# Kernel tuning notes

Hardware: AMD Instinct MI355X
Metric: run time of the kernel (lower is better)

The kernel has to match this reference:

```python
import jax, jax.numpy as jnp
import numpy as np

N_NODES = 50000
N_EDGES = 800000
D_IN = 64
F1 = 64
F2 = 64
D_HID = 100


def setup_inputs() -> dict:
    key = jax.random.key(0)
    ks = jax.random.split(key, 12)
    x = jax.random.normal(ks[0], (N_NODES, D_IN), dtype=jnp.float32)
    edge_src = jax.random.randint(ks[1], (N_EDGES,), 0, N_NODES, dtype=jnp.int32)
    edge_dst = jax.random.randint(ks[2], (N_EDGES,), 0, N_NODES, dtype=jnp.int32)
    # stands in for pre-normalized GCN adjacency values (D^-1/2 (A+I) D^-1/2)
    edge_weight = jax.random.uniform(ks[3], (N_EDGES,), dtype=jnp.float32)
    def glorot(k, shape):
        lim = np.sqrt(6.0 / (shape[0] + shape[1]))
        return jax.random.uniform(k, shape, jnp.float32, -lim, lim)
    W1 = glorot(ks[4], (D_IN, F1))
    b1 = jnp.zeros((F1,), jnp.float32)
    W2 = glorot(ks[5], (F1, F2))
    b2 = jnp.zeros((F2,), jnp.float32)
    Wd = glorot(ks[6], (F2, D_HID))
    bd = jnp.zeros((D_HID,), jnp.float32)
    Wo = glorot(ks[7], (D_HID, 1))
    bo = jnp.zeros((1,), jnp.float32)
    return {"x": x, "edge_src": edge_src, "edge_dst": edge_dst,
            "edge_weight": edge_weight, "W1": W1, "b1": b1, "W2": W2,
            "b2": b2, "Wd": Wd, "bd": bd, "Wo": Wo, "bo": bo}


def _gcn_conv(x, edge_src, edge_dst, edge_weight, W, b):
    # spektral GCNConv: out = swish(A_norm @ (X @ W) + b)
    h = x @ W                                        # [N, F]
    msg = h[edge_src] * edge_weight[:, None]          # [E, F] gather + scale
    agg = jax.ops.segment_sum(msg, edge_dst, num_segments=N_NODES)  # [N, F]
    return jax.nn.swish(agg + b)


def reference(x, edge_src, edge_dst, edge_weight, W1, b1, W2, b2, Wd, bd, Wo, bo):
    h = _gcn_conv(x, edge_src, edge_dst, edge_weight, W1, b1)
    h = _gcn_conv(h, edge_src, edge_dst, edge_weight, W2, b2)
    h = jax.nn.swish(h @ Wd + bd)                    # Dense(100, swish)
    return jax.nn.sigmoid(h @ Wo + bo)               # Dense(1, sigmoid) -> [N, 1]
```

## Files before the change

### kernel.cpp

```cpp
#include <hip/hip_runtime.h>
#include <hip/hip_fp16.h>

#define N_NODES 50000
#define N_EDGES 800000
#define D 64
#define DHID 100
#define NTILES (N_NODES / 16)
#define NCT 7
#define CAP 64
#define FILL_BLOCKS ((N_EDGES + 255) / 256)
#define MM_BLOCKS ((NTILES + 3) / 4)

typedef unsigned short ushort;
typedef unsigned int uint;
typedef __attribute__((ext_vector_type(8))) short s16x8;
typedef __attribute__((ext_vector_type(4))) float f32x4;

#define MFMA16(A, B, C) __builtin_amdgcn_mfma_f32_16x16x32_bf16((A), (B), (C), 0, 0, 0)

__device__ __forceinline__ float swishf(float x) { return x / (1.0f + __expf(-x)); }

__device__ __forceinline__ ushort f2bf(float f) {
    uint u = __float_as_uint(f);
    uint r = (u + 0x7fffu + ((u >> 16) & 1u)) >> 16;
    return (ushort)r;
}
__device__ __forceinline__ float bf2f(ushort h) { return __uint_as_float((uint)h << 16); }
__device__ __forceinline__ float bf_lo(uint d) { return __uint_as_float(d << 16); }
__device__ __forceinline__ float bf_hi(uint d) { return __uint_as_float(d & 0xffff0000u); }

__device__ __forceinline__ void accum8(float* acc, uint4 v, float w) {
    acc[0] = fmaf(w, bf_lo(v.x), acc[0]);
    acc[1] = fmaf(w, bf_hi(v.x), acc[1]);
    acc[2] = fmaf(w, bf_lo(v.y), acc[2]);
    acc[3] = fmaf(w, bf_hi(v.y), acc[3]);
    acc[4] = fmaf(w, bf_lo(v.z), acc[4]);
    acc[5] = fmaf(w, bf_hi(v.z), acc[5]);
    acc[6] = fmaf(w, bf_lo(v.w), acc[6]);
    acc[7] = fmaf(w, bf_hi(v.w), acc[7]);
}

__global__ __launch_bounds__(256) void fill_and_l1(const int* __restrict__ src,
                                                   const int* __restrict__ dst,
                                                   const float* __restrict__ w,
                                                   int* __restrict__ degPad,
                                                   uint* __restrict__ csr,
                                                   const float* __restrict__ X,
                                                   const float* __restrict__ W,
                                                   ushort* __restrict__ H) {
    __shared__ __align__(16) short sBT[2][D][72];
    __shared__ __align__(16) short rep[4][16][72];
    int tid = threadIdx.x;

    if (blockIdx.x < FILL_BLOCKS) {
        int e = blockIdx.x * 256 + tid;
        if (e < N_EDGES) {
            int d = dst[e];
            uint hw = (uint)__half_as_ushort(__float2half_rn(w[e]));
            uint payload = (uint)src[e] | (hw << 16);
            int r = atomicAdd(&degPad[d << 4], 1);
            r = min(r, CAP - 1);
            csr[(d << 6) + r] = payload;
        }
        return;
    }

    for (int idx = tid; idx < D * D; idx += 256) {
        int k = idx >> 6, c = idx & 63;
        float wv = W[idx];
        ushort hi = f2bf(wv);
        ushort lo = f2bf(wv - bf2f(hi));
        sBT[0][c][k] = (short)hi;
        sBT[1][c][k] = (short)lo;
    }
    __syncthreads();
    int wv_ = tid >> 6, lane = tid & 63, quad = lane >> 4, m = lane & 15;
    int tile = (blockIdx.x - FILL_BLOCKS) * 4 + wv_;
    if (tile >= NTILES) return;
    int node0 = tile * 16;

    f32x4 acc[4] = {{0,0,0,0},{0,0,0,0},{0,0,0,0},{0,0,0,0}};
#pragma unroll
    for (int kt = 0; kt < 2; ++kt) {
        int k0 = kt * 32 + quad * 8;
        const float* xp = X + ((size_t)(node0 + m) << 6) + k0;
        float4 xa = *((const float4*)xp);
        float4 xb = *((const float4*)(xp + 4));
        float xv[8] = {xa.x, xa.y, xa.z, xa.w, xb.x, xb.y, xb.z, xb.w};
        s16x8 ahi, alo;
#pragma unroll
        for (int jj = 0; jj < 8; ++jj) {
            ushort hi = f2bf(xv[jj]);
            ahi[jj] = (short)hi;
            alo[jj] = (short)f2bf(xv[jj] - bf2f(hi));
        }
#pragma unroll
        for (int ct = 0; ct < 4; ++ct) {
            int n = ct * 16 + m;
            s16x8 bhi = *((const s16x8*)&sBT[0][n][k0]);
            s16x8 blo = *((const s16x8*)&sBT[1][n][k0]);
            acc[ct] = MFMA16(ahi, bhi, acc[ct]);
            acc[ct] = MFMA16(ahi, blo, acc[ct]);
            acc[ct] = MFMA16(alo, bhi, acc[ct]);
        }
    }
#pragma unroll
    for (int ct = 0; ct < 4; ++ct)
#pragma unroll
        for (int r = 0; r < 4; ++r)
            rep[wv_][quad * 4 + r][ct * 16 + m] = (short)f2bf(acc[ct][r]);
#pragma unroll
    for (int half = 0; half < 2; ++half) {
        int r = (lane >> 3) + half * 8;
        int c0 = (lane & 7) * 8;
        s16x8 v = *((const s16x8*)&rep[wv_][r][c0]);
        *((s16x8*)(H + ((size_t)(node0 + r) << 6) + c0)) = v;
    }
}

__global__ __launch_bounds__(256) void mfma_l2(const ushort* __restrict__ act,
                                               const float* __restrict__ W,
                                               ushort* __restrict__ H) {
    __shared__ __align__(16) short sBT[2][D][72];
    __shared__ __align__(16) short rep[4][16][72];
    int tid = threadIdx.x;
    for (int idx = tid; idx < D * D; idx += 256) {
        int k = idx >> 6, c = idx & 63;
        float wv = W[idx];
        ushort hi = f2bf(wv);
        ushort lo = f2bf(wv - bf2f(hi));
        sBT[0][c][k] = (short)hi;
        sBT[1][c][k] = (short)lo;
    }
    __syncthreads();
    int w = tid >> 6, lane = tid & 63, quad = lane >> 4, m = lane & 15;
    int tile = blockIdx.x * 4 + w;
    if (tile >= NTILES) return;
    int node0 = tile * 16;

    f32x4 acc[4] = {{0,0,0,0},{0,0,0,0},{0,0,0,0},{0,0,0,0}};
#pragma unroll
    for (int kt = 0; kt < 2; ++kt) {
        int k0 = kt * 32 + quad * 8;
        s16x8 a = *((const s16x8*)(act + ((size_t)(node0 + m) << 6) + k0));
#pragma unroll
        for (int ct = 0; ct < 4; ++ct) {
            int n = ct * 16 + m;
            s16x8 bhi = *((const s16x8*)&sBT[0][n][k0]);
            s16x8 blo = *((const s16x8*)&sBT[1][n][k0]);
            acc[ct] = MFMA16(a, bhi, acc[ct]);
            acc[ct] = MFMA16(a, blo, acc[ct]);
        }
    }
#pragma unroll
    for (int ct = 0; ct < 4; ++ct)
#pragma unroll
        for (int r = 0; r < 4; ++r)
            rep[w][quad * 4 + r][ct * 16 + m] = (short)f2bf(acc[ct][r]);
#pragma unroll
    for (int half = 0; half < 2; ++half) {
        int r = (lane >> 3) + half * 8;
        int c0 = (lane & 7) * 8;
        s16x8 v = *((const s16x8*)&rep[w][r][c0]);
        *((s16x8*)(H + ((size_t)(node0 + r) << 6) + c0)) = v;
    }
}

__global__ __launch_bounds__(256) void gather_act(const ushort* __restrict__ H,
                                                  const int* __restrict__ degPad,
                                                  const uint* __restrict__ csr,
                                                  const float* __restrict__ bias,
                                                  ushort* __restrict__ actOut) {
    int tid = threadIdx.x;
    int wave = tid >> 6, lane = tid & 63;
    int j = lane >> 3, fg = lane & 7;
    int node = blockIdx.x * 4 + wave;
    int cnt = (degPad[node << 4] + 31) & ~31;
    const uint* bucket = csr + ((size_t)node << 6);

    float acc[8] = {0, 0, 0, 0, 0, 0, 0, 0};
    for (int base = 0; base < cnt; base += 32) {
        int i0 = base + j;
        uint e0 = bucket[i0];
        uint e1 = bucket[i0 + 8];
        uint e2 = bucket[i0 + 16];
        uint e3 = bucket[i0 + 24];
        float w0 = __half2float(__ushort_as_half((ushort)(e0 >> 16)));
        float w1 = __half2float(__ushort_as_half((ushort)(e1 >> 16)));
        float w2 = __half2float(__ushort_as_half((ushort)(e2 >> 16)));
        float w3 = __half2float(__ushort_as_half((ushort)(e3 >> 16)));
        uint4 v0 = *((const uint4*)(H + ((size_t)(e0 & 0xffffu) << 6) + (fg << 3)));
        uint4 v1 = *((const uint4*)(H + ((size_t)(e1 & 0xffffu) << 6) + (fg << 3)));
        uint4 v2 = *((const uint4*)(H + ((size_t)(e2 & 0xffffu) << 6) + (fg << 3)));
        uint4 v3 = *((const uint4*)(H + ((size_t)(e3 & 0xffffu) << 6) + (fg << 3)));
        accum8(acc, v0, w0);
        accum8(acc, v1, w1);
        accum8(acc, v2, w2);
        accum8(acc, v3, w3);
    }
#pragma unroll
    for (int t = 0; t < 8; ++t) {
        acc[t] += __shfl_xor(acc[t], 8, 64);
        acc[t] += __shfl_xor(acc[t], 16, 64);
        acc[t] += __shfl_xor(acc[t], 32, 64);
    }
    if (j == 0) {
        float4 ba = ((const float4*)bias)[fg * 2];
        float4 bb = ((const float4*)bias)[fg * 2 + 1];
        float r0 = swishf(acc[0] + ba.x);
        float r1 = swishf(acc[1] + ba.y);
        float r2 = swishf(acc[2] + ba.z);
        float r3 = swishf(acc[3] + ba.w);
        float r4 = swishf(acc[4] + bb.x);
        float r5 = swishf(acc[5] + bb.y);
        float r6 = swishf(acc[6] + bb.z);
        float r7 = swishf(acc[7] + bb.w);
        uint4 u;
        u.x = (uint)f2bf(r0) | ((uint)f2bf(r1) << 16);
        u.y = (uint)f2bf(r2) | ((uint)f2bf(r3) << 16);
        u.z = (uint)f2bf(r4) | ((uint)f2bf(r5) << 16);
        u.w = (uint)f2bf(r6) | ((uint)f2bf(r7) << 16);
        *((uint4*)(actOut + ((size_t)node << 6) + (fg << 3))) = u;
    }
}

__global__ __launch_bounds__(256) void mfma_head(const ushort* __restrict__ act2,
                                                 const float* __restrict__ Wd,
                                                 const float* __restrict__ bd,
                                                 const float* __restrict__ Wo,
                                                 const float* __restrict__ bo,
                                                 float* __restrict__ out) {
    __shared__ __align__(16) short sBT[2][NCT * 16][72];
    __shared__ float sbd[NCT * 16];
    __shared__ float sWo[NCT * 16];
    int tid = threadIdx.x;
    for (int idx = tid; idx < NCT * 16 * D; idx += 256) {
        int jj = idx >> 6, k = idx & 63;
        float wv = (jj < DHID) ? Wd[k * DHID + jj] : 0.f;
        ushort hi = f2bf(wv);
        ushort lo = f2bf(wv - bf2f(hi));
        sBT[0][jj][k] = (short)hi;
        sBT[1][jj][k] = (short)lo;
    }
    if (tid < NCT * 16) {
        sbd[tid] = (tid < DHID) ? bd[tid] : 0.f;
        sWo[tid] = (tid < DHID) ? Wo[tid] : 0.f;
    }
    __syncthreads();
    int w = tid >> 6, lane = tid & 63, quad = lane >> 4, m = lane & 15;
    int tile = blockIdx.x * 4 + w;
    if (tile >= NTILES) return;
    int node0 = tile * 16;

    f32x4 acc[NCT];
#pragma unroll
    for (int ct = 0; ct < NCT; ++ct) acc[ct] = (f32x4){0, 0, 0, 0};
#pragma unroll
    for (int kt = 0; kt < 2; ++kt) {
        int k0 = kt * 32 + quad * 8;
        s16x8 a = *((const s16x8*)(act2 + ((size_t)(node0 + m) << 6) + k0));
#pragma unroll
        for (int ct = 0; ct < NCT; ++ct) {
            int n = ct * 16 + m;
            s16x8 bhi = *((const s16x8*)&sBT[0][n][k0]);
            s16x8 blo = *((const s16x8*)&sBT[1][n][k0]);
            acc[ct] = MFMA16(a, bhi, acc[ct]);
            acc[ct] = MFMA16(a, blo, acc[ct]);
        }
    }
    float part[4] = {0, 0, 0, 0};
#pragma unroll
    for (int ct = 0; ct < NCT; ++ct) {
        int jj = ct * 16 + m;
        float bdv = sbd[jj], wov = sWo[jj];
#pragma unroll
        for (int r = 0; r < 4; ++r)
            part[r] = fmaf(swishf(acc[ct][r] + bdv), wov, part[r]);
    }
#pragma unroll
    for (int r = 0; r < 4; ++r) {
        part[r] += __shfl_xor(part[r], 1, 64);
        part[r] += __shfl_xor(part[r], 2, 64);
        part[r] += __shfl_xor(part[r], 4, 64);
        part[r] += __shfl_xor(part[r], 8, 64);
    }
    if (m == 0) {
        float b0 = bo[0];
        float4 o;
        o.x = 1.f / (1.f + __expf(-(part[0] + b0)));
        o.y = 1.f / (1.f + __expf(-(part[1] + b0)));
        o.z = 1.f / (1.f + __expf(-(part[2] + b0)));
        o.w = 1.f / (1.f + __expf(-(part[3] + b0)));
        *((float4*)(out + node0 + quad * 4)) = o;
    }
}

extern "C" void kernel_launch(void* const* d_in, const int* in_sizes, int n_in,
                              void* d_out, int out_size, void* d_ws, size_t ws_size,
                              hipStream_t stream) {
    const float* x   = (const float*)d_in[0];
    const int* esrc  = (const int*)d_in[1];
    const int* edst  = (const int*)d_in[2];
    const float* ew  = (const float*)d_in[3];
    const float* W1  = (const float*)d_in[4];
    const float* b1  = (const float*)d_in[5];
    const float* W2  = (const float*)d_in[6];
    const float* b2  = (const float*)d_in[7];
    const float* Wd  = (const float*)d_in[8];
    const float* bd  = (const float*)d_in[9];
    const float* Wo  = (const float*)d_in[10];
    const float* bo  = (const float*)d_in[11];
    float* out = (float*)d_out;

    char* ws = (char*)d_ws;
    ushort* H1   = (ushort*)ws;  ws += (size_t)N_NODES * D * sizeof(ushort);
    ushort* act1 = (ushort*)ws;  ws += (size_t)N_NODES * D * sizeof(ushort);
    ushort* H2   = (ushort*)ws;  ws += (size_t)N_NODES * D * sizeof(ushort);
    ushort* act2 = (ushort*)ws;  ws += (size_t)N_NODES * D * sizeof(ushort);
    uint* csr    = (uint*)ws;    ws += (size_t)N_NODES * CAP * sizeof(uint);
    int* degPad  = (int*)ws;     ws += (size_t)N_NODES * 16 * sizeof(int);

    const int gBlocks = N_NODES / 4;

    hipMemsetAsync(csr, 0, (size_t)N_NODES * (CAP + 16) * sizeof(uint), stream);

    fill_and_l1<<<FILL_BLOCKS + MM_BLOCKS, 256, 0, stream>>>(esrc, edst, ew, degPad, csr,
                                                             x, W1, H1);

    gather_act<<<gBlocks, 256, 0, stream>>>(H1, degPad, csr, b1, act1);

    mfma_l2<<<(NTILES + 3) / 4, 256, 0, stream>>>(act1, W2, H2);
    gather_act<<<gBlocks, 256, 0, stream>>>(H2, degPad, csr, b2, act2);

    mfma_head<<<(NTILES + 3) / 4, 256, 0, stream>>>(act2, Wd, bd, Wo, bo, out);
}
```

Before: 215.3 us.

## Fuse all stages into one persistent cooperative kernel with grid syncs

Replaces the memset and five separate kernel launches with a single cooperative persistent kernel. Inside it, grid.sync separates the stages: zeroing, edge bucketing plus layer-1 matmul, gather, layer-2 matmul, gather, and the head. Degree counters are packed densely instead of padded to 16 ints each. This removes launch gaps and the separate memset, at the cost of grid-wide barriers, fewer resident waves during the latency-bound gather stages, and occupancy capped by the shared-memory and register use of the fused kernel.

```diff
diff --git a/kernel.cpp b/kernel.cpp
--- a/kernel.cpp
+++ b/kernel.cpp
@@ -1,5 +1,8 @@
 #include <hip/hip_runtime.h>
 #include <hip/hip_fp16.h>
+#include <hip/hip_cooperative_groups.h>
+
+namespace cg = cooperative_groups;
 
 #define N_NODES 50000
 #define N_EDGES 800000
@@ -8,8 +11,7 @@
 #define NTILES (N_NODES / 16)
 #define NCT 7
 #define CAP 64
-#define FILL_BLOCKS ((N_EDGES + 255) / 256)
-#define MM_BLOCKS ((NTILES + 3) / 4)
+#define ZERO_UINT4 812500
 
 typedef unsigned short ushort;
 typedef unsigned int uint;
@@ -40,258 +42,270 @@
     acc[7] = fmaf(w, bf_hi(v.w), acc[7]);
 }
 
-__global__ __launch_bounds__(256) void fill_and_l1(const int* __restrict__ src,
-                                                   const int* __restrict__ dst,
-                                                   const float* __restrict__ w,
-                                                   int* __restrict__ degPad,
-                                                   uint* __restrict__ csr,
-                                                   const float* __restrict__ X,
-                                                   const float* __restrict__ W,
-                                                   ushort* __restrict__ H) {
-    __shared__ __align__(16) short sBT[2][D][72];
-    __shared__ __align__(16) short rep[4][16][72];
-    int tid = threadIdx.x;
-
-    if (blockIdx.x < FILL_BLOCKS) {
-        int e = blockIdx.x * 256 + tid;
-        if (e < N_EDGES) {
-            int d = dst[e];
-            uint hw = (uint)__half_as_ushort(__float2half_rn(w[e]));
-            uint payload = (uint)src[e] | (hw << 16);
-            int r = atomicAdd(&degPad[d << 4], 1);
-            r = min(r, CAP - 1);
-            csr[(d << 6) + r] = payload;
-        }
-        return;
-    }
-
-    for (int idx = tid; idx < D * D; idx += 256) {
-        int k = idx >> 6, c = idx & 63;
-        float wv = W[idx];
-        ushort hi = f2bf(wv);
-        ushort lo = f2bf(wv - bf2f(hi));
-        sBT[0][c][k] = (short)hi;
-        sBT[1][c][k] = (short)lo;
-    }
-    __syncthreads();
-    int wv_ = tid >> 6, lane = tid & 63, quad = lane >> 4, m = lane & 15;
-    int tile = (blockIdx.x - FILL_BLOCKS) * 4 + wv_;
-    if (tile >= NTILES) return;
-    int node0 = tile * 16;
-
-    f32x4 acc[4] = {{0,0,0,0},{0,0,0,0},{0,0,0,0},{0,0,0,0}};
-#pragma unroll
-    for (int kt = 0; kt < 2; ++kt) {
-        int k0 = kt * 32 + quad * 8;
-        const float* xp = X + ((size_t)(node0 + m) << 6) + k0;
-        float4 xa = *((const float4*)xp);
-        float4 xb = *((const float4*)(xp + 4));
-        float xv[8] = {xa.x, xa.y, xa.z, xa.w, xb.x, xb.y, xb.z, xb.w};
-        s16x8 ahi, alo;
-#pragma unroll
-        for (int jj = 0; jj < 8; ++jj) {
-            ushort hi = f2bf(xv[jj]);
-            ahi[jj] = (short)hi;
-            alo[jj] = (short)f2bf(xv[jj] - bf2f(hi));
-        }
-#pragma unroll
-        for (int ct = 0; ct < 4; ++ct) {
-            int n = ct * 16 + m;
-            s16x8 bhi = *((const s16x8*)&sBT[0][n][k0]);
-            s16x8 blo = *((const s16x8*)&sBT[1][n][k0]);
-            acc[ct] = MFMA16(ahi, bhi, acc[ct]);
-            acc[ct] = MFMA16(ahi, blo, acc[ct]);
-            acc[ct] = MFMA16(alo, bhi, acc[ct]);
-        }
-    }
-#pragma unroll
-    for (int ct = 0; ct < 4; ++ct)
-#pragma unroll
-        for (int r = 0; r < 4; ++r)
-            rep[wv_][quad * 4 + r][ct * 16 + m] = (short)f2bf(acc[ct][r]);
-#pragma unroll
-    for (int half = 0; half < 2; ++half) {
-        int r = (lane >> 3) + half * 8;
-        int c0 = (lane & 7) * 8;
-        s16x8 v = *((const s16x8*)&rep[wv_][r][c0]);
-        *((s16x8*)(H + ((size_t)(node0 + r) << 6) + c0)) = v;
-    }
-}
-
-__global__ __launch_bounds__(256) void mfma_l2(const ushort* __restrict__ act,
-                                               const float* __restrict__ W,
-                                               ushort* __restrict__ H) {
-    __shared__ __align__(16) short sBT[2][D][72];
-    __shared__ __align__(16) short rep[4][16][72];
-    int tid = threadIdx.x;
-    for (int idx = tid; idx < D * D; idx += 256) {
-        int k = idx >> 6, c = idx & 63;
-        float wv = W[idx];
-        ushort hi = f2bf(wv);
-        ushort lo = f2bf(wv - bf2f(hi));
-        sBT[0][c][k] = (short)hi;
-        sBT[1][c][k] = (short)lo;
-    }
-    __syncthreads();
-    int w = tid >> 6, lane = tid & 63, quad = lane >> 4, m = lane & 15;
-    int tile = blockIdx.x * 4 + w;
-    if (tile >= NTILES) return;
-    int node0 = tile * 16;
-
-    f32x4 acc[4] = {{0,0,0,0},{0,0,0,0},{0,0,0,0},{0,0,0,0}};
-#pragma unroll
-    for (int kt = 0; kt < 2; ++kt) {
-        int k0 = kt * 32 + quad * 8;
-        s16x8 a = *((const s16x8*)(act + ((size_t)(node0 + m) << 6) + k0));
-#pragma unroll
-        for (int ct = 0; ct < 4; ++ct) {
-            int n = ct * 16 + m;
-            s16x8 bhi = *((const s16x8*)&sBT[0][n][k0]);
-            s16x8 blo = *((const s16x8*)&sBT[1][n][k0]);
-            acc[ct] = MFMA16(a, bhi, acc[ct]);
-            acc[ct] = MFMA16(a, blo, acc[ct]);
-        }
-    }
-#pragma unroll
-    for (int ct = 0; ct < 4; ++ct)
-#pragma unroll
-        for (int r = 0; r < 4; ++r)
-            rep[w][quad * 4 + r][ct * 16 + m] = (short)f2bf(acc[ct][r]);
-#pragma unroll
-    for (int half = 0; half < 2; ++half) {
-        int r = (lane >> 3) + half * 8;
-        int c0 = (lane & 7) * 8;
-        s16x8 v = *((const s16x8*)&rep[w][r][c0]);
-        *((s16x8*)(H + ((size_t)(node0 + r) << 6) + c0)) = v;
-    }
-}
-
-__global__ __launch_bounds__(256) void gather_act(const ushort* __restrict__ H,
-                                                  const int* __restrict__ degPad,
-                                                  const uint* __restrict__ csr,
-                                                  const float* __restrict__ bias,
-                                                  ushort* __restrict__ actOut) {
-    int tid = threadIdx.x;
-    int wave = tid >> 6, lane = tid & 63;
+__device__ __forceinline__ void gather_stage(const ushort* __restrict__ H,
+                                             const int* __restrict__ deg,
+                                             const uint* __restrict__ csr,
+                                             const float* __restrict__ bias,
+                                             ushort* __restrict__ actOut,
+                                             int waveslot, int nslots, int lane) {
     int j = lane >> 3, fg = lane & 7;
-    int node = blockIdx.x * 4 + wave;
-    int cnt = (degPad[node << 4] + 31) & ~31;
-    const uint* bucket = csr + ((size_t)node << 6);
-
-    float acc[8] = {0, 0, 0, 0, 0, 0, 0, 0};
-    for (int base = 0; base < cnt; base += 32) {
-        int i0 = base + j;
-        uint e0 = bucket[i0];
-        uint e1 = bucket[i0 + 8];
-        uint e2 = bucket[i0 + 16];
-        uint e3 = bucket[i0 + 24];
-        float w0 = __half2float(__ushort_as_half((ushort)(e0 >> 16)));
-        float w1 = __half2float(__ushort_as_half((ushort)(e1 >> 16)));
-        float w2 = __half2float(__ushort_as_half((ushort)(e2 >> 16)));
-        float w3 = __half2float(__ushort_as_half((ushort)(e3 >> 16)));
-        uint4 v0 = *((const uint4*)(H + ((size_t)(e0 & 0xffffu) << 6) + (fg << 3)));
-        uint4 v1 = *((const uint4*)(H + ((size_t)(e1 & 0xffffu) << 6) + (fg << 3)));
-        uint4 v2 = *((const uint4*)(H + ((size_t)(e2 & 0xffffu) << 6) + (fg << 3)));
-        uint4 v3 = *((const uint4*)(H + ((size_t)(e3 & 0xffffu) << 6) + (fg << 3)));
-        accum8(acc, v0, w0);
-        accum8(acc, v1, w1);
-        accum8(acc, v2, w2);
-        accum8(acc, v3, w3);
-    }
-#pragma unroll
-    for (int t = 0; t < 8; ++t) {
-        acc[t] += __shfl_xor(acc[t], 8, 64);
-        acc[t] += __shfl_xor(acc[t], 16, 64);
-        acc[t] += __shfl_xor(acc[t], 32, 64);
-    }
-    if (j == 0) {
-        float4 ba = ((const float4*)bias)[fg * 2];
-        float4 bb = ((const float4*)bias)[fg * 2 + 1];
-        float r0 = swishf(acc[0] + ba.x);
-        float r1 = swishf(acc[1] + ba.y);
-        float r2 = swishf(acc[2] + ba.z);
-        float r3 = swishf(acc[3] + ba.w);
-        float r4 = swishf(acc[4] + bb.x);
-        float r5 = swishf(acc[5] + bb.y);
-        float r6 = swishf(acc[6] + bb.z);
-        float r7 = swishf(acc[7] + bb.w);
-        uint4 u;
-        u.x = (uint)f2bf(r0) | ((uint)f2bf(r1) << 16);
-        u.y = (uint)f2bf(r2) | ((uint)f2bf(r3) << 16);
-        u.z = (uint)f2bf(r4) | ((uint)f2bf(r5) << 16);
-        u.w = (uint)f2bf(r6) | ((uint)f2bf(r7) << 16);
-        *((uint4*)(actOut + ((size_t)node << 6) + (fg << 3))) = u;
-    }
-}
-
-__global__ __launch_bounds__(256) void mfma_head(const ushort* __restrict__ act2,
-                                                 const float* __restrict__ Wd,
-                                                 const float* __restrict__ bd,
-                                                 const float* __restrict__ Wo,
-                                                 const float* __restrict__ bo,
-                                                 float* __restrict__ out) {
-    __shared__ __align__(16) short sBT[2][NCT * 16][72];
-    __shared__ float sbd[NCT * 16];
-    __shared__ float sWo[NCT * 16];
-    int tid = threadIdx.x;
-    for (int idx = tid; idx < NCT * 16 * D; idx += 256) {
-        int jj = idx >> 6, k = idx & 63;
-        float wv = (jj < DHID) ? Wd[k * DHID + jj] : 0.f;
-        ushort hi = f2bf(wv);
-        ushort lo = f2bf(wv - bf2f(hi));
-        sBT[0][jj][k] = (short)hi;
-        sBT[1][jj][k] = (short)lo;
-    }
-    if (tid < NCT * 16) {
-        sbd[tid] = (tid < DHID) ? bd[tid] : 0.f;
-        sWo[tid] = (tid < DHID) ? Wo[tid] : 0.f;
-    }
-    __syncthreads();
-    int w = tid >> 6, lane = tid & 63, quad = lane >> 4, m = lane & 15;
-    int tile = blockIdx.x * 4 + w;
-    if (tile >= NTILES) return;
-    int node0 = tile * 16;
-
-    f32x4 acc[NCT];
-#pragma unroll
-    for (int ct = 0; ct < NCT; ++ct) acc[ct] = (f32x4){0, 0, 0, 0};
-#pragma unroll
-    for (int kt = 0; kt < 2; ++kt) {
-        int k0 = kt * 32 + quad * 8;
-        s16x8 a = *((const s16x8*)(act2 + ((size_t)(node0 + m) << 6) + k0));
-#pragma unroll
-        for (int ct = 0; ct < NCT; ++ct) {
-            int n = ct * 16 + m;
-            s16x8 bhi = *((const s16x8*)&sBT[0][n][k0]);
-            s16x8 blo = *((const s16x8*)&sBT[1][n][k0]);
-            acc[ct] = MFMA16(a, bhi, acc[ct]);
-            acc[ct] = MFMA16(a, blo, acc[ct]);
-        }
-    }
-    float part[4] = {0, 0, 0, 0};
-#pragma unroll
-    for (int ct = 0; ct < NCT; ++ct) {
-        int jj = ct * 16 + m;
-        float bdv = sbd[jj], wov = sWo[jj];
-#pragma unroll
-        for (int r = 0; r < 4; ++r)
-            part[r] = fmaf(swishf(acc[ct][r] + bdv), wov, part[r]);
-    }
-#pragma unroll
-    for (int r = 0; r < 4; ++r) {
-        part[r] += __shfl_xor(part[r], 1, 64);
-        part[r] += __shfl_xor(part[r], 2, 64);
-        part[r] += __shfl_xor(part[r], 4, 64);
-        part[r] += __shfl_xor(part[r], 8, 64);
-    }
-    if (m == 0) {
+    float4 ba = ((const float4*)bias)[fg * 2];
+    float4 bb = ((const float4*)bias)[fg * 2 + 1];
+    for (int node = waveslot; node < N_NODES; node += nslots) {
+        int cnt = min((deg[node] + 31) & ~31, CAP);
+        const uint* bucket = csr + ((size_t)node << 6);
+        float acc[8] = {0, 0, 0, 0, 0, 0, 0, 0};
+        for (int base = 0; base < cnt; base += 32) {
+            int i0 = base + j;
+            uint e0 = bucket[i0];
+            uint e1 = bucket[i0 + 8];
+            uint e2 = bucket[i0 + 16];
+            uint e3 = bucket[i0 + 24];
+            float w0 = __half2float(__ushort_as_half((ushort)(e0 >> 16)));
+            float w1 = __half2float(__ushort_as_half((ushort)(e1 >> 16)));
+            float w2 = __half2float(__ushort_as_half((ushort)(e2 >> 16)));
+            float w3 = __half2float(__ushort_as_half((ushort)(e3 >> 16)));
+            uint4 v0 = *((const uint4*)(H + ((size_t)(e0 & 0xffffu) << 6) + (fg << 3)));
+            uint4 v1 = *((const uint4*)(H + ((size_t)(e1 & 0xffffu) << 6) + (fg << 3)));
+            uint4 v2 = *((const uint4*)(H + ((size_t)(e2 & 0xffffu) << 6) + (fg << 3)));
+            uint4 v3 = *((const uint4*)(H + ((size_t)(e3 & 0xffffu) << 6) + (fg << 3)));
+            accum8(acc, v0, w0);
+            accum8(acc, v1, w1);
+            accum8(acc, v2, w2);
+            accum8(acc, v3, w3);
+        }
+#pragma unroll
+        for (int t = 0; t < 8; ++t) {
+            acc[t] += __shfl_xor(acc[t], 8, 64);
+            acc[t] += __shfl_xor(acc[t], 16, 64);
+            acc[t] += __shfl_xor(acc[t], 32, 64);
+        }
+        if (j == 0) {
+            float r0 = swishf(acc[0] + ba.x);
+            float r1 = swishf(acc[1] + ba.y);
+            float r2 = swishf(acc[2] + ba.z);
+            float r3 = swishf(acc[3] + ba.w);
+            float r4 = swishf(acc[4] + bb.x);
+            float r5 = swishf(acc[5] + bb.y);
+            float r6 = swishf(acc[6] + bb.z);
+            float r7 = swishf(acc[7] + bb.w);
+            uint4 u;
+            u.x = (uint)f2bf(r0) | ((uint)f2bf(r1) << 16);
+            u.y = (uint)f2bf(r2) | ((uint)f2bf(r3) << 16);
+            u.z = (uint)f2bf(r4) | ((uint)f2bf(r5) << 16);
+            u.w = (uint)f2bf(r6) | ((uint)f2bf(r7) << 16);
+            *((uint4*)(actOut + ((size_t)node << 6) + (fg << 3))) = u;
+        }
+    }
+}
+
+__global__ void __launch_bounds__(256) mega(const int* __restrict__ src,
+                                            const int* __restrict__ dst,
+                                            const float* __restrict__ ew,
+                                            const float* __restrict__ X,
+                                            const float* __restrict__ W1,
+                                            const float* __restrict__ b1,
+                                            const float* __restrict__ W2,
+                                            const float* __restrict__ b2,
+                                            const float* __restrict__ Wd,
+                                            const float* __restrict__ bd,
+                                            const float* __restrict__ Wo,
+                                            const float* __restrict__ bo,
+                                            uint* __restrict__ csr,
+                                            int* __restrict__ deg,
+                                            ushort* __restrict__ H1,
+                                            ushort* __restrict__ act1,
+                                            ushort* __restrict__ H2,
+                                            ushort* __restrict__ act2,
+                                            float* __restrict__ out) {
+    __shared__ __align__(16) char smem[33280];
+    cg::grid_group grid = cg::this_grid();
+    const int tid = threadIdx.x;
+    const int gtid = blockIdx.x * 256 + tid;
+    const int gsize = gridDim.x * 256;
+    const int wv = tid >> 6, lane = tid & 63;
+    const int quad = lane >> 4, m = lane & 15;
+    const int waveslot = blockIdx.x * 4 + wv;
+    const int nslots = gridDim.x * 4;
+
+    {
+        uint4 z = {0, 0, 0, 0};
+        uint4* p = (uint4*)csr;
+        for (int i = gtid; i < ZERO_UINT4; i += gsize) p[i] = z;
+    }
+    grid.sync();
+
+    for (int e = gtid; e < N_EDGES; e += gsize) {
+        int d = dst[e];
+        uint hw = (uint)__half_as_ushort(__float2half_rn(ew[e]));
+        uint payload = (uint)src[e] | (hw << 16);
+        int r = atomicAdd(&deg[d], 1);
+        r = min(r, CAP - 1);
+        csr[(d << 6) + r] = payload;
+    }
+    {
+        short (*sBT)[D][72] = (short(*)[D][72])smem;
+        short (*rep)[16][72] = (short(*)[16][72])(smem + 18432);
+        for (int idx = tid; idx < D * D; idx += 256) {
+            int k = idx >> 6, c = idx & 63;
+            float wt = W1[idx];
+            ushort hi = f2bf(wt);
+            sBT[0][c][k] = (short)hi;
+            sBT[1][c][k] = (short)f2bf(wt - bf2f(hi));
+        }
+        __syncthreads();
+        for (int tile = waveslot; tile < NTILES; tile += nslots) {
+            int node0 = tile * 16;
+            f32x4 acc[4] = {{0,0,0,0},{0,0,0,0},{0,0,0,0},{0,0,0,0}};
+#pragma unroll
+            for (int kt = 0; kt < 2; ++kt) {
+                int k0 = kt * 32 + quad * 8;
+                const float* xp = X + ((size_t)(node0 + m) << 6) + k0;
+                float4 xa = *((const float4*)xp);
+                float4 xb = *((const float4*)(xp + 4));
+                float xv[8] = {xa.x, xa.y, xa.z, xa.w, xb.x, xb.y, xb.z, xb.w};
+                s16x8 ahi, alo;
+#pragma unroll
+                for (int jj = 0; jj < 8; ++jj) {
+                    ushort hi = f2bf(xv[jj]);
+                    ahi[jj] = (short)hi;
+                    alo[jj] = (short)f2bf(xv[jj] - bf2f(hi));
+                }
+#pragma unroll
+                for (int ct = 0; ct < 4; ++ct) {
+                    int n = ct * 16 + m;
+                    s16x8 bhi = *((const s16x8*)&sBT[0][n][k0]);
+                    s16x8 blo = *((const s16x8*)&sBT[1][n][k0]);
+                    acc[ct] = MFMA16(ahi, bhi, acc[ct]);
+                    acc[ct] = MFMA16(ahi, blo, acc[ct]);
+                    acc[ct] = MFMA16(alo, bhi, acc[ct]);
+                }
+            }
+#pragma unroll
+            for (int ct = 0; ct < 4; ++ct)
+#pragma unroll
+                for (int r = 0; r < 4; ++r)
+                    rep[wv][quad * 4 + r][ct * 16 + m] = (short)f2bf(acc[ct][r]);
+#pragma unroll
+            for (int half = 0; half < 2; ++half) {
+                int r = (lane >> 3) + half * 8;
+                int c0 = (lane & 7) * 8;
+                s16x8 v = *((const s16x8*)&rep[wv][r][c0]);
+                *((s16x8*)(H1 + ((size_t)(node0 + r) << 6) + c0)) = v;
+            }
+        }
+    }
+    grid.sync();
+
+    gather_stage(H1, deg, csr, b1, act1, waveslot, nslots, lane);
+    grid.sync();
+
+    {
+        short (*sBT)[D][72] = (short(*)[D][72])smem;
+        short (*rep)[16][72] = (short(*)[16][72])(smem + 18432);
+        for (int idx = tid; idx < D * D; idx += 256) {
+            int k = idx >> 6, c = idx & 63;
+            float wt = W2[idx];
+            ushort hi = f2bf(wt);
+            sBT[0][c][k] = (short)hi;
+            sBT[1][c][k] = (short)f2bf(wt - bf2f(hi));
+        }
+        __syncthreads();
+        for (int tile = waveslot; tile < NTILES; tile += nslots) {
+            int node0 = tile * 16;
+            f32x4 acc[4] = {{0,0,0,0},{0,0,0,0},{0,0,0,0},{0,0,0,0}};
+#pragma unroll
+            for (int kt = 0; kt < 2; ++kt) {
+                int k0 = kt * 32 + quad * 8;
+                s16x8 a = *((const s16x8*)(act1 + ((size_t)(node0 + m) << 6) + k0));
+#pragma unroll
+                for (int ct = 0; ct < 4; ++ct) {
+                    int n = ct * 16 + m;
+                    s16x8 bhi = *((const s16x8*)&sBT[0][n][k0]);
+                    s16x8 blo = *((const s16x8*)&sBT[1][n][k0]);
+                    acc[ct] = MFMA16(a, bhi, acc[ct]);
+                    acc[ct] = MFMA16(a, blo, acc[ct]);
+                }
+            }
+#pragma unroll
+            for (int ct = 0; ct < 4; ++ct)
+#pragma unroll
+                for (int r = 0; r < 4; ++r)
+                    rep[wv][quad * 4 + r][ct * 16 + m] = (short)f2bf(acc[ct][r]);
+#pragma unroll
+            for (int half = 0; half < 2; ++half) {
+                int r = (lane >> 3) + half * 8;
+                int c0 = (lane & 7) * 8;
+                s16x8 v = *((const s16x8*)&rep[wv][r][c0]);
+                *((s16x8*)(H2 + ((size_t)(node0 + r) << 6) + c0)) = v;
+            }
+        }
+    }
+    grid.sync();
+
+    gather_stage(H2, deg, csr, b2, act2, waveslot, nslots, lane);
+    grid.sync();
+
+    {
+        short (*sBT)[NCT * 16][72] = (short(*)[NCT * 16][72])smem;
+        float* sbd = (float*)(smem + 32256);
+        float* sWo = (float*)(smem + 32256 + 448);
+        for (int idx = tid; idx < NCT * 16 * D; idx += 256) {
+            int jj = idx >> 6, k = idx & 63;
+            float wt = (jj < DHID) ? Wd[k * DHID + jj] : 0.f;
+            ushort hi = f2bf(wt);
+            sBT[0][jj][k] = (short)hi;
+            sBT[1][jj][k] = (short)f2bf(wt - bf2f(hi));
+        }
+        if (tid < NCT * 16) {
+            sbd[tid] = (tid < DHID) ? bd[tid] : 0.f;
+            sWo[tid] = (tid < DHID) ? Wo[tid] : 0.f;
+        }
+        __syncthreads();
         float b0 = bo[0];
-        float4 o;
-        o.x = 1.f / (1.f + __expf(-(part[0] + b0)));
-        o.y = 1.f / (1.f + __expf(-(part[1] + b0)));
-        o.z = 1.f / (1.f + __expf(-(part[2] + b0)));
-        o.w = 1.f / (1.f + __expf(-(part[3] + b0)));
-        *((float4*)(out + node0 + quad * 4)) = o;
+        for (int tile = waveslot; tile < NTILES; tile += nslots) {
+            int node0 = tile * 16;
+            f32x4 acc[NCT];
+#pragma unroll
+            for (int ct = 0; ct < NCT; ++ct) acc[ct] = (f32x4){0, 0, 0, 0};
+#pragma unroll
+            for (int kt = 0; kt < 2; ++kt) {
+                int k0 = kt * 32 + quad * 8;
+                s16x8 a = *((const s16x8*)(act2 + ((size_t)(node0 + m) << 6) + k0));
+#pragma unroll
+                for (int ct = 0; ct < NCT; ++ct) {
+                    int n = ct * 16 + m;
+                    s16x8 bhi = *((const s16x8*)&sBT[0][n][k0]);
+                    s16x8 blo = *((const s16x8*)&sBT[1][n][k0]);
+                    acc[ct] = MFMA16(a, bhi, acc[ct]);
+                    acc[ct] = MFMA16(a, blo, acc[ct]);
+                }
+            }
+            float part[4] = {0, 0, 0, 0};
+#pragma unroll
+            for (int ct = 0; ct < NCT; ++ct) {
+                int jj = ct * 16 + m;
+                float bdv = sbd[jj], wov = sWo[jj];
+#pragma unroll
+                for (int r = 0; r < 4; ++r)
+                    part[r] = fmaf(swishf(acc[ct][r] + bdv), wov, part[r]);
+            }
+#pragma unroll
+            for (int r = 0; r < 4; ++r) {
+                part[r] += __shfl_xor(part[r], 1, 64);
+                part[r] += __shfl_xor(part[r], 2, 64);
+                part[r] += __shfl_xor(part[r], 4, 64);
+                part[r] += __shfl_xor(part[r], 8, 64);
+            }
+            if (m == 0) {
+                float4 o;
+                o.x = 1.f / (1.f + __expf(-(part[0] + b0)));
+                o.y = 1.f / (1.f + __expf(-(part[1] + b0)));
+                o.z = 1.f / (1.f + __expf(-(part[2] + b0)));
+                o.w = 1.f / (1.f + __expf(-(part[3] + b0)));
+                *((float4*)(out + node0 + quad * 4)) = o;
+            }
+        }
     }
 }
 
@@ -318,19 +332,23 @@
     ushort* H2   = (ushort*)ws;  ws += (size_t)N_NODES * D * sizeof(ushort);
     ushort* act2 = (ushort*)ws;  ws += (size_t)N_NODES * D * sizeof(ushort);
     uint* csr    = (uint*)ws;    ws += (size_t)N_NODES * CAP * sizeof(uint);
-    int* degPad  = (int*)ws;     ws += (size_t)N_NODES * 16 * sizeof(int);
-
-    const int gBlocks = N_NODES / 4;
-
-    hipMemsetAsync(csr, 0, (size_t)N_NODES * (CAP + 16) * sizeof(uint), stream);
-
-    fill_and_l1<<<FILL_BLOCKS + MM_BLOCKS, 256, 0, stream>>>(esrc, edst, ew, degPad, csr,
-                                                             x, W1, H1);
-
-    gather_act<<<gBlocks, 256, 0, stream>>>(H1, degPad, csr, b1, act1);
-
-    mfma_l2<<<(NTILES + 3) / 4, 256, 0, stream>>>(act1, W2, H2);
-    gather_act<<<gBlocks, 256, 0, stream>>>(H2, degPad, csr, b2, act2);
-
-    mfma_head<<<(NTILES + 3) / 4, 256, 0, stream>>>(act2, Wd, bd, Wo, bo, out);
-}
+    int* deg     = (int*)ws;     ws += (size_t)N_NODES * sizeof(int);
+
+    int maxB = 0;
+    if (hipOccupancyMaxActiveBlocksPerMultiprocessor(&maxB, mega, 256, 0) != hipSuccess || maxB < 1)
+        maxB = 2;
+    int dev = 0, numCU = 256;
+    hipGetDevice(&dev);
+    hipDeviceGetAttribute(&numCU, hipDeviceAttributeMultiprocessorCount, dev);
+    int grid = maxB * numCU;
+
+    void* args[] = {
+        (void*)&esrc, (void*)&edst, (void*)&ew,
+        (void*)&x, (void*)&W1, (void*)&b1, (void*)&W2, (void*)&b2,
+        (void*)&Wd, (void*)&bd, (void*)&Wo, (void*)&bo,
+        (void*)&csr, (void*)&deg,
+        (void*)&H1, (void*)&act1, (void*)&H2, (void*)&act2,
+        (void*)&out
+    };
+    hipLaunchCooperativeKernel((const void*)mega, dim3(grid), dim3(256), args, 0, stream);
+}
```

Result: slower. 470.2 us (+118.3%).

## Partition CSR fill by destination range and pack degree counters densely

Applied to the files above, without the earlier changes.

The edge-fill phase now uses 8 groups × 390 slices. Every block scans a strided slice of all edges and handles only those whose destination falls in its group's node range. The aim is to localize atomics and CSR scatter writes to one region per group, for better L2 locality. Degree counters are packed densely instead of padded to 64 bytes, which shrinks the memset but brings false sharing on atomics back. The cost is that each edge's dst is read 8 times, and the gather count is now clamped to CAP.

```diff
diff --git a/kernel.cpp b/kernel.cpp
--- a/kernel.cpp
+++ b/kernel.cpp
@@ -8,8 +8,11 @@
 #define NTILES (N_NODES / 16)
 #define NCT 7
 #define CAP 64
-#define FILL_BLOCKS ((N_EDGES + 255) / 256)
+#define NGROUPS 8
+#define NSLICES 390
+#define FILL_BLOCKS (NGROUPS * NSLICES)
 #define MM_BLOCKS ((NTILES + 3) / 4)
+#define DST_PER_GROUP (N_NODES / NGROUPS)
 
 typedef unsigned short ushort;
 typedef unsigned int uint;
@@ -43,7 +46,7 @@
 __global__ __launch_bounds__(256) void fill_and_l1(const int* __restrict__ src,
                                                    const int* __restrict__ dst,
                                                    const float* __restrict__ w,
-                                                   int* __restrict__ degPad,
+                                                   int* __restrict__ deg,
                                                    uint* __restrict__ csr,
                                                    const float* __restrict__ X,
                                                    const float* __restrict__ W,
@@ -53,14 +56,19 @@
     int tid = threadIdx.x;
 
     if (blockIdx.x < FILL_BLOCKS) {
-        int e = blockIdx.x * 256 + tid;
-        if (e < N_EDGES) {
+        const int g = blockIdx.x & (NGROUPS - 1);
+        const int s = blockIdx.x >> 3;
+        const int lo = g * DST_PER_GROUP;
+        const int hi = lo + DST_PER_GROUP;
+        for (int e = s * 256 + tid; e < N_EDGES; e += NSLICES * 256) {
             int d = dst[e];
-            uint hw = (uint)__half_as_ushort(__float2half_rn(w[e]));
-            uint payload = (uint)src[e] | (hw << 16);
-            int r = atomicAdd(&degPad[d << 4], 1);
-            r = min(r, CAP - 1);
-            csr[(d << 6) + r] = payload;
+            if (d >= lo && d < hi) {
+                uint hw = (uint)__half_as_ushort(__float2half_rn(w[e]));
+                uint payload = (uint)src[e] | (hw << 16);
+                int r = atomicAdd(&deg[d], 1);
+                r = min(r, CAP - 1);
+                csr[(d << 6) + r] = payload;
+            }
         }
         return;
     }
@@ -69,9 +77,8 @@
         int k = idx >> 6, c = idx & 63;
         float wv = W[idx];
         ushort hi = f2bf(wv);
-        ushort lo = f2bf(wv - bf2f(hi));
         sBT[0][c][k] = (short)hi;
-        sBT[1][c][k] = (short)lo;
+        sBT[1][c][k] = (short)f2bf(wv - bf2f(hi));
     }
     __syncthreads();
     int wv_ = tid >> 6, lane = tid & 63, quad = lane >> 4, m = lane & 15;
@@ -128,9 +135,8 @@
         int k = idx >> 6, c = idx & 63;
         float wv = W[idx];
         ushort hi = f2bf(wv);
-        ushort lo = f2bf(wv - bf2f(hi));
         sBT[0][c][k] = (short)hi;
-        sBT[1][c][k] = (short)lo;
+        sBT[1][c][k] = (short)f2bf(wv - bf2f(hi));
     }
     __syncthreads();
     int w = tid >> 6, lane = tid & 63, quad = lane >> 4, m = lane & 15;
@@ -167,7 +173,7 @@
 }
 
 __global__ __launch_bounds__(256) void gather_act(const ushort* __restrict__ H,
-                                                  const int* __restrict__ degPad,
+                                                  const int* __restrict__ deg,
                                                   const uint* __restrict__ csr,
                                                   const float* __restrict__ bias,
                                                   ushort* __restrict__ actOut) {
@@ -175,7 +181,7 @@
     int wave = tid >> 6, lane = tid & 63;
     int j = lane >> 3, fg = lane & 7;
     int node = blockIdx.x * 4 + wave;
-    int cnt = (degPad[node << 4] + 31) & ~31;
+    int cnt = min((deg[node] + 31) & ~31, CAP);
     const uint* bucket = csr + ((size_t)node << 6);
 
     float acc[8] = {0, 0, 0, 0, 0, 0, 0, 0};
@@ -238,9 +244,8 @@
         int jj = idx >> 6, k = idx & 63;
         float wv = (jj < DHID) ? Wd[k * DHID + jj] : 0.f;
         ushort hi = f2bf(wv);
-        ushort lo = f2bf(wv - bf2f(hi));
         sBT[0][jj][k] = (short)hi;
-        sBT[1][jj][k] = (short)lo;
+        sBT[1][jj][k] = (short)f2bf(wv - bf2f(hi));
     }
     if (tid < NCT * 16) {
         sbd[tid] = (tid < DHID) ? bd[tid] : 0.f;
@@ -318,19 +323,19 @@
     ushort* H2   = (ushort*)ws;  ws += (size_t)N_NODES * D * sizeof(ushort);
     ushort* act2 = (ushort*)ws;  ws += (size_t)N_NODES * D * sizeof(ushort);
     uint* csr    = (uint*)ws;    ws += (size_t)N_NODES * CAP * sizeof(uint);
-    int* degPad  = (int*)ws;     ws += (size_t)N_NODES * 16 * sizeof(int);
+    int* deg     = (int*)ws;     ws += (size_t)N_NODES * sizeof(int);
 
     const int gBlocks = N_NODES / 4;
 
-    hipMemsetAsync(csr, 0, (size_t)N_NODES * (CAP + 16) * sizeof(uint), stream);
-
-    fill_and_l1<<<FILL_BLOCKS + MM_BLOCKS, 256, 0, stream>>>(esrc, edst, ew, degPad, csr,
+    hipMemsetAsync(csr, 0, (size_t)N_NODES * (CAP + 1) * sizeof(uint), stream);
+
+    fill_and_l1<<<FILL_BLOCKS + MM_BLOCKS, 256, 0, stream>>>(esrc, edst, ew, deg, csr,
                                                              x, W1, H1);
 
-    gather_act<<<gBlocks, 256, 0, stream>>>(H1, degPad, csr, b1, act1);
+    gather_act<<<gBlocks, 256, 0, stream>>>(H1, deg, csr, b1, act1);
 
     mfma_l2<<<(NTILES + 3) / 4, 256, 0, stream>>>(act1, W2, H2);
-    gather_act<<<gBlocks, 256, 0, stream>>>(H2, degPad, csr, b2, act2);
+    gather_act<<<gBlocks, 256, 0, stream>>>(H2, deg, csr, b2, act2);
 
     mfma_head<<<(NTILES + 3) / 4, 256, 0, stream>>>(act2, Wd, bd, Wo, bo, out);
 }
```

Result: faster. 201.4 us (-6.5%).
